# Performance work log

Hardware: AMD Instinct MI355X
Metric: run time of the kernel (lower is better)

The kernel has to match this reference:

```python
import jax, jax.numpy as jnp
import numpy as np

N = 100000
E = 1_600_000
IN = 128
HID = 32
HEADS = 4
OUT = 2
NEG_SLOPE = 0.2  # PyG GATv2Conv default negative_slope


def setup_inputs() -> dict:
    key = jax.random.key(0)
    ks = jax.random.split(key, 18)
    g = lambda k, shape, fan: jax.random.normal(k, shape, dtype=jnp.float32) / np.sqrt(fan)
    return {
        "x": jax.random.normal(ks[0], (N, IN), dtype=jnp.float32),
        "edge_index": jax.random.randint(ks[1], (2, E), 0, N, dtype=jnp.int32),
        # conv1: GATv2Conv(IN, HID, heads=HEADS)
        "W1l": g(ks[2], (IN, HEADS * HID), IN),
        "b1l": jnp.zeros((HEADS * HID,), jnp.float32),
        "W1r": g(ks[3], (IN, HEADS * HID), IN),
        "b1r": jnp.zeros((HEADS * HID,), jnp.float32),
        "att1": g(ks[4], (HEADS, HID), HID),
        "bias1": jnp.zeros((HEADS * HID,), jnp.float32),
        # conv2: GATv2Conv(HEADS*HID, HID, heads=1)
        "W2l": g(ks[5], (HEADS * HID, HID), HEADS * HID),
        "b2l": jnp.zeros((HID,), jnp.float32),
        "W2r": g(ks[6], (HEADS * HID, HID), HEADS * HID),
        "b2r": jnp.zeros((HID,), jnp.float32),
        "att2": g(ks[7], (1, HID), HID),
        "bias2": jnp.zeros((HID,), jnp.float32),
        # final linear
        "Wlin": g(ks[8], (HID, OUT), HID),
        "blin": jnp.zeros((OUT,), jnp.float32),
    }


def _gatv2(x, src, dst, Wl, bl, Wr, br, att, bias, heads, ch):
    n = x.shape[0]
    xl = (x @ Wl + bl).reshape(n, heads, ch)  # source transform
    xr = (x @ Wr + br).reshape(n, heads, ch)  # target transform
    # GATv2 edge score: a^T LeakyReLU(xl_j + xr_i)
    e = jax.nn.leaky_relu(xl[src] + xr[dst], NEG_SLOPE)      # [E, H, C]
    score = jnp.einsum('ehc,hc->eh', e, att)                  # [E, H]
    # segment softmax over edges sharing a destination node
    m = jax.ops.segment_max(score, dst, num_segments=n)
    ex = jnp.exp(score - m[dst])
    denom = jax.ops.segment_sum(ex, dst, num_segments=n)
    alpha = ex / denom[dst]                                   # [E, H]
    out = jax.ops.segment_sum(alpha[..., None] * xl[src], dst, num_segments=n)
    return out.reshape(n, heads * ch) + bias


def reference(x, edge_index, W1l, b1l, W1r, b1r, att1, bias1,
              W2l, b2l, W2r, b2r, att2, bias2, Wlin, blin):
    # add self-loops (PyG GATv2Conv default add_self_loops=True)
    loop = jnp.arange(N, dtype=edge_index.dtype)
    src = jnp.concatenate([edge_index[0], loop])
    dst = jnp.concatenate([edge_index[1], loop])

    h = _gatv2(x, src, dst, W1l, b1l, W1r, b1r, att1, bias1, HEADS, HID)
    h = jax.nn.elu(h)
    # dropout is inactive in eval mode
    h = _gatv2(h, src, dst, W2l, b2l, W2r, b2r, att2, bias2, 1, HID)
    h = jax.nn.elu(h)
    return h @ Wlin + blin  # [N, OUT]
```

## Files before the change

### kernel.cpp

```cpp
#include <hip/hip_runtime.h>
#include <hip/hip_fp16.h>
#include <math.h>

#define N_NODES 100000
#define E_EDGES 1600000
#define ETOT (E_EDGES + N_NODES)
#define NEG 0.2f
#define NB 782
#define BCAP 2560
#define CHUNK 8192
#define NCHB ((ETOT + CHUNK - 1) / CHUNK)
#define GEMM1_BLOCKS ((N_NODES + 63) / 64)

typedef _Float16 half8 __attribute__((ext_vector_type(8)));
typedef _Float16 half4v __attribute__((ext_vector_type(4)));
typedef _Float16 half2v __attribute__((ext_vector_type(2)));
typedef float floatx4 __attribute__((ext_vector_type(4)));

union H8I {
  half8 v;
  _Float16 e[8];
  int i[4];
};

__device__ __forceinline__ float elu(float v) { return v > 0.f ? v : (__expf(v) - 1.f); }

__device__ __forceinline__ float score8(half8 a, half8 r, half8 av) {
  half8 t = a + r;
  t = __builtin_elementwise_max(t, t * (_Float16)NEG);
  half8 s8 = t * av;
  half4v s4 = __builtin_shufflevector(s8, s8, 0, 1, 2, 3) +
              __builtin_shufflevector(s8, s8, 4, 5, 6, 7);
  half2v s2 = __builtin_shufflevector(s4, s4, 0, 1) +
              __builtin_shufflevector(s4, s4, 2, 3);
  return (float)s2[0] + (float)s2[1];
}

__global__ __launch_bounds__(256) void fusedA_kernel(
    const int* __restrict__ ei, unsigned* __restrict__ cursor,
    unsigned* __restrict__ bins,
    const float* __restrict__ W1l, const float* __restrict__ W1r,
    const float* __restrict__ b1l, const float* __restrict__ b1r,
    const float* __restrict__ W2l, const float* __restrict__ W2r,
    const float* __restrict__ b2l, const float* __restrict__ b2r,
    const float* __restrict__ att1, const float* __restrict__ att2,
    _Float16* __restrict__ Bperm, _Float16* __restrict__ B2perm,
    float* __restrict__ biascat, float* __restrict__ bias2cat,
    _Float16* __restrict__ att1h, _Float16* __restrict__ att2h) {
  int t = threadIdx.x;
  if (blockIdx.x < NCHB) {
    __shared__ unsigned cnt[NB];
    __shared__ unsigned base[NB];
    for (int b = t; b < NB; b += 256) cnt[b] = 0;
    __syncthreads();
    int e0 = blockIdx.x * CHUNK;
    int dstr[CHUNK / 256];
#pragma unroll
    for (int i = 0; i < CHUNK / 256; i++) {
      int e = e0 + i * 256 + t;
      int dst = 0;
      if (e < ETOT) {
        dst = (e < E_EDGES) ? ei[E_EDGES + e] : (e - E_EDGES);
        atomicAdd(&cnt[dst >> 7], 1u);
      }
      dstr[i] = dst;
    }
    __syncthreads();
    for (int b = t; b < NB; b += 256) {
      unsigned c = cnt[b];
      base[b] = c ? atomicAdd(&cursor[b], c) : 0u;
      cnt[b] = 0;
    }
    __syncthreads();
#pragma unroll
    for (int i = 0; i < CHUNK / 256; i++) {
      int e = e0 + i * 256 + t;
      if (e < ETOT) {
        int dst = dstr[i];
        int src = (e < E_EDGES) ? ei[e] : dst;
        int b = dst >> 7;
        unsigned off = atomicAdd(&cnt[b], 1u);
        bins[(size_t)b * BCAP + base[b] + off] =
            ((unsigned)(dst & 127) << 17) | (unsigned)src;
      }
    }
  } else {
    int pb = blockIdx.x - NCHB;
    int gt = pb * 256 + t;
    int gstr = 20 * 256;
    for (int e = gt; e < 4096; e += gstr) {
      int nt = e >> 8, kt = (e >> 6) & 3, lane = e & 63;
      int n = nt * 16 + (lane & 15);
      int kb = kt * 32 + (lane >> 4) * 8;
#pragma unroll
      for (int j = 0; j < 8; j++) {
        int k = kb + j;
        float val = (n < 128) ? W1l[k * 128 + n] : W1r[k * 128 + (n - 128)];
        Bperm[(size_t)e * 8 + j] = (_Float16)val;
      }
    }
    for (int e = gt; e < 1024; e += gstr) {
      int nt = e >> 8, kt = (e >> 6) & 3, lane = e & 63;
      int n = nt * 16 + (lane & 15);
      int kb = kt * 32 + (lane >> 4) * 8;
#pragma unroll
      for (int j = 0; j < 8; j++) {
        int k = kb + j;
        float val = (n < 32) ? W2l[k * 32 + n] : W2r[k * 32 + (n - 32)];
        B2perm[(size_t)e * 8 + j] = (_Float16)val;
      }
    }
    if (pb == 0) {
      biascat[t] = (t < 128) ? b1l[t] : b1r[t - 128];
      if (t < 64) bias2cat[t] = (t < 32) ? b2l[t] : b2r[t - 32];
      if (t < 128) att1h[t] = (_Float16)att1[t];
      if (t < 32) att2h[t] = (_Float16)att2[t];
    }
  }
}

__global__ __launch_bounds__(1024) void scan_buckets(const unsigned* __restrict__ cursor,
                                                     unsigned* __restrict__ bucket_base,
                                                     unsigned* __restrict__ rowptr) {
  __shared__ unsigned s[1024];
  int t = threadIdx.x;
  unsigned v = (t < NB) ? cursor[t] : 0u;
  s[t] = v;
  __syncthreads();
  for (int off = 1; off < 1024; off <<= 1) {
    unsigned a = (t >= off) ? s[t - off] : 0u;
    __syncthreads();
    s[t] += a;
    __syncthreads();
  }
  if (t < NB) bucket_base[t] = s[t] - v;
  if (t == 0) { bucket_base[NB] = ETOT; rowptr[N_NODES] = ETOT; }
}

__global__ __launch_bounds__(256) void fusedB_kernel(
    const unsigned* __restrict__ bins, const unsigned* __restrict__ cursor,
    const unsigned* __restrict__ bucket_base,
    unsigned* __restrict__ rowptr, int* __restrict__ csr_src,
    const float* __restrict__ x, const _Float16* __restrict__ Bperm,
    const float* __restrict__ biascat,
    __half* __restrict__ xlh, __half* __restrict__ xrh) {
  __shared__ __align__(16) char smem[64 * 256];
  int t = threadIdx.x;
  if (blockIdx.x < NB) {
    unsigned* cnt = (unsigned*)smem;
    unsigned* pref = cnt + 128;
    int b = blockIdx.x;
    unsigned cntb = cursor[b];
    unsigned bbase = bucket_base[b];
    const unsigned* bp = bins + (size_t)b * BCAP;
    if (t < 128) cnt[t] = 0;
    __syncthreads();
    for (unsigned i = t; i < cntb; i += 256) atomicAdd(&cnt[bp[i] >> 17], 1u);
    __syncthreads();
    if (t < 128) pref[t] = cnt[t];
    __syncthreads();
    for (int off = 1; off < 128; off <<= 1) {
      unsigned a = (t >= off && t < 128) ? pref[t - off] : 0u;
      __syncthreads();
      if (t < 128) pref[t] += a;
      __syncthreads();
    }
    if (t < 128) {
      unsigned excl = pref[t] - cnt[t];
      pref[t] = excl;
      int n = (b << 7) + t;
      if (n < N_NODES) rowptr[n] = bbase + excl;
      cnt[t] = 0;
    }
    __syncthreads();
    for (unsigned i = t; i < cntb; i += 256) {
      unsigned en = bp[i];
      int j = (int)(en >> 17);
      unsigned off = atomicAdd(&cnt[j], 1u);
      csr_src[bbase + pref[j] + off] = (int)(en & 0x1FFFFu);
    }
  } else {
    int base = (blockIdx.x - NB) * 64;
    {
      int row = t >> 2, c4 = t & 3;
      int grow = base + row;
      const float* gp = x + (size_t)grow * 128 + c4 * 32;
#pragma unroll
      for (int j = 0; j < 4; j++) {
        half8 v = {};
        if (grow < N_NODES) {
          float4 f0 = *(const float4*)(gp + j * 8);
          float4 f1 = *(const float4*)(gp + j * 8 + 4);
          v[0] = (_Float16)f0.x; v[1] = (_Float16)f0.y;
          v[2] = (_Float16)f0.z; v[3] = (_Float16)f0.w;
          v[4] = (_Float16)f1.x; v[5] = (_Float16)f1.y;
          v[6] = (_Float16)f1.z; v[7] = (_Float16)f1.w;
        }
        int off = row * 256 + ((((c4 * 4 + j) * 16)) ^ ((row & 7) << 4));
        *(half8*)(smem + off) = v;
      }
    }
    int wid = t >> 6, lane = t & 63;
    half8 bf[4][4];
#pragma unroll
    for (int ntl = 0; ntl < 4; ntl++)
#pragma unroll
      for (int kt = 0; kt < 4; kt++) {
        int f = (wid * 4 + ntl) * 4 + kt;
        bf[ntl][kt] = *(const half8*)(Bperm + ((size_t)f * 64 + lane) * 8);
      }
    floatx4 acc[4][4] = {};
    __syncthreads();
#pragma unroll
    for (int kt = 0; kt < 4; kt++) {
      half8 a[4];
#pragma unroll
      for (int mt = 0; mt < 4; mt++) {
        int row = mt * 16 + (lane & 15);
        int kchunk = kt * 4 + (lane >> 4);
        int off = row * 256 + ((kchunk * 16) ^ ((row & 7) << 4));
        a[mt] = *(const half8*)(smem + off);
      }
#pragma unroll
      for (int mt = 0; mt < 4; mt++)
#pragma unroll
        for (int ntl = 0; ntl < 4; ntl++)
          acc[mt][ntl] = __builtin_amdgcn_mfma_f32_16x16x32_f16(a[mt], bf[ntl][kt],
                                                                acc[mt][ntl], 0, 0, 0);
    }
#pragma unroll
    for (int mt = 0; mt < 4; mt++) {
#pragma unroll
      for (int i = 0; i < 4; i++) {
        int row = base + mt * 16 + (lane >> 4) * 4 + i;
        if (row >= N_NODES) continue;
#pragma unroll
        for (int ntl = 0; ntl < 4; ntl++) {
          int col = wid * 64 + ntl * 16 + (lane & 15);
          float v = acc[mt][ntl][i] + biascat[col];
          if (col < 128) xlh[(size_t)row * 128 + col] = __float2half_rn(v);
          else xrh[(size_t)row * 128 + (col - 128)] = __float2half_rn(v);
        }
      }
    }
  }
}

__global__ __launch_bounds__(256) void gemm2_mfma(
    const __half* __restrict__ h1h, const _Float16* __restrict__ B2perm,
    const float* __restrict__ bias2cat,
    __half* __restrict__ xl2h, __half* __restrict__ xr2h) {
  __shared__ __align__(16) char smem[64 * 256];
  int t = threadIdx.x;
  int base = blockIdx.x * 64;
  {
    int row = t >> 2, c4 = t & 3;
    int grow = base + row;
    const char* gp = (const char*)(h1h + (size_t)grow * 128 + c4 * 32);
#pragma unroll
    for (int j = 0; j < 4; j++) {
      half8 v = {};
      if (grow < N_NODES) v = *(const half8*)(gp + j * 16);
      int off = row * 256 + ((((c4 * 4 + j) * 16)) ^ ((row & 7) << 4));
      *(half8*)(smem + off) = v;
    }
  }
  int wid = t >> 6, lane = t & 63;
  half8 bf[4];
#pragma unroll
  for (int kt = 0; kt < 4; kt++) {
    int f = wid * 4 + kt;
    bf[kt] = *(const half8*)(B2perm + ((size_t)f * 64 + lane) * 8);
  }
  floatx4 acc[4] = {};
  __syncthreads();
#pragma unroll
  for (int kt = 0; kt < 4; kt++) {
    half8 a[4];
#pragma unroll
    for (int mt = 0; mt < 4; mt++) {
      int row = mt * 16 + (lane & 15);
      int kchunk = kt * 4 + (lane >> 4);
      int off = row * 256 + ((kchunk * 16) ^ ((row & 7) << 4));
      a[mt] = *(const half8*)(smem + off);
    }
#pragma unroll
    for (int mt = 0; mt < 4; mt++)
      acc[mt] = __builtin_amdgcn_mfma_f32_16x16x32_f16(a[mt], bf[kt], acc[mt], 0, 0, 0);
  }
  int col = wid * 16 + (lane & 15);
  float bv = bias2cat[col];
#pragma unroll
  for (int mt = 0; mt < 4; mt++) {
#pragma unroll
    for (int i = 0; i < 4; i++) {
      int row = base + mt * 16 + (lane >> 4) * 4 + i;
      if (row >= N_NODES) continue;
      float v = acc[mt][i] + bv;
      if (col < 32) xl2h[(size_t)row * 32 + col] = __float2half_rn(v);
      else xr2h[(size_t)row * 32 + (col - 32)] = __float2half_rn(v);
    }
  }
}

__global__ __launch_bounds__(256) void l1_gather_kernel(
    const __half* __restrict__ xlh, const __half* __restrict__ xrh,
    const int* __restrict__ csr_src, const unsigned* __restrict__ rowptr,
    const _Float16* __restrict__ att1h, const float* __restrict__ bias,
    __half* __restrict__ h1h) {
  int wid = threadIdx.x >> 6;
  int lane = threadIdx.x & 63;
  int n = blockIdx.x * 4 + wid;
  if (n >= N_NODES) return;
  int g = lane >> 4;
  int q = lane & 15;
  int c0 = q * 8;
  half8 rv = *(const half8*)(xrh + (size_t)n * 128 + c0);
  half8 av = *(const half8*)(att1h + c0);
  unsigned beg = rowptr[n], end = rowptr[n + 1];
  int nit = (int)(end - beg + 3) >> 2;
  float d = 0.f;
  H8I acc;
  acc.v = (half8){};
  for (int i = 0; i < nit; i++) {
    unsigned e = beg + i * 4 + g;
    bool valid = e < end;
    int s = csr_src[valid ? e : (end - 1)];
    H8I a;
    a.v = *(const half8*)(xlh + (size_t)s * 128 + c0);
    float v = score8(a.v, rv, av);
    v += __shfl_xor(v, 1);
    v += __shfl_xor(v, 2);
    float p = valid ? __expf(v - 4.f) : 0.f;
    d += p;
    _Float16 ph = (_Float16)p;
    half8 p8 = {ph, ph, ph, ph, ph, ph, ph, ph};
    acc.v = p8 * a.v + acc.v;
  }
#pragma unroll
  for (int msk = 16; msk <= 32; msk <<= 1) {
    d += __shfl_xor(d, msk);
    H8I o;
#pragma unroll
    for (int k = 0; k < 4; k++) o.i[k] = __shfl_xor(acc.i[k], msk);
    acc.v = acc.v + o.v;
  }
  if (g == 0) {
    float inv = 1.f / d;
    H8I res;
#pragma unroll
    for (int j = 0; j < 8; j++)
      res.e[j] = (_Float16)elu((float)acc.e[j] * inv + bias[c0 + j]);
    *(half8*)(h1h + (size_t)n * 128 + c0) = res.v;
  }
}

__global__ __launch_bounds__(256) void l2_gather_kernel(
    const __half* __restrict__ xl2h, const __half* __restrict__ xr2h,
    const int* __restrict__ csr_src, const unsigned* __restrict__ rowptr,
    const _Float16* __restrict__ att2h, const float* __restrict__ bias,
    const float* __restrict__ Wlin, const float* __restrict__ blin,
    float* __restrict__ out) {
  int wid = threadIdx.x >> 6;
  int lane = threadIdx.x & 63;
  int n = blockIdx.x * 4 + wid;
  if (n >= N_NODES) return;
  int g = lane >> 2;
  int q = lane & 3;
  int c0 = q * 8;
  half8 rv = *(const half8*)(xr2h + (size_t)n * 32 + c0);
  half8 av = *(const half8*)(att2h + c0);
  unsigned beg = rowptr[n], end = rowptr[n + 1];
  int nit = (int)(end - beg + 15) >> 4;
  float d = 0.f;
  H8I acc;
  acc.v = (half8){};
  for (int i = 0; i < nit; i++) {
    unsigned e = beg + i * 16 + g;
    bool valid = e < end;
    int s = csr_src[valid ? e : (end - 1)];
    H8I a;
    a.v = *(const half8*)(xl2h + (size_t)s * 32 + c0);
    float v = score8(a.v, rv, av);
    v += __shfl_xor(v, 1);
    v += __shfl_xor(v, 2);
    float p = valid ? __expf(v - 4.f) : 0.f;
    d += p;
    _Float16 ph = (_Float16)p;
    half8 p8 = {ph, ph, ph, ph, ph, ph, ph, ph};
    acc.v = p8 * a.v + acc.v;
  }
#pragma unroll
  for (int msk = 4; msk <= 32; msk <<= 1) {
    d += __shfl_xor(d, msk);
    H8I o;
#pragma unroll
    for (int k = 0; k < 4; k++) o.i[k] = __shfl_xor(acc.i[k], msk);
    acc.v = acc.v + o.v;
  }
  float inv = 1.f / d;
  float o0 = 0.f, o1 = 0.f;
#pragma unroll
  for (int j = 0; j < 8; j++) {
    float v = elu((float)acc.e[j] * inv + bias[c0 + j]);
    o0 = fmaf(v, Wlin[(c0 + j) * 2 + 0], o0);
    o1 = fmaf(v, Wlin[(c0 + j) * 2 + 1], o1);
  }
  o0 += __shfl_xor(o0, 1); o1 += __shfl_xor(o1, 1);
  o0 += __shfl_xor(o0, 2); o1 += __shfl_xor(o1, 2);
  if (lane == 0) {
    out[(size_t)n * 2 + 0] = o0 + blin[0];
    out[(size_t)n * 2 + 1] = o1 + blin[1];
  }
}

extern "C" void kernel_launch(void* const* d_in, const int* in_sizes, int n_in,
                              void* d_out, int out_size, void* d_ws, size_t ws_size,
                              hipStream_t stream) {
  const float* x     = (const float*)d_in[0];
  const int*   ei    = (const int*)d_in[1];
  const float* W1l   = (const float*)d_in[2];
  const float* b1l   = (const float*)d_in[3];
  const float* W1r   = (const float*)d_in[4];
  const float* b1r   = (const float*)d_in[5];
  const float* att1  = (const float*)d_in[6];
  const float* bias1 = (const float*)d_in[7];
  const float* W2l   = (const float*)d_in[8];
  const float* b2l   = (const float*)d_in[9];
  const float* W2r   = (const float*)d_in[10];
  const float* b2r   = (const float*)d_in[11];
  const float* att2  = (const float*)d_in[12];
  const float* bias2 = (const float*)d_in[13];
  const float* Wlin  = (const float*)d_in[14];
  const float* blin  = (const float*)d_in[15];
  float* out = (float*)d_out;

  __half* xl1h  = (__half*)d_ws;
  __half* xr1h  = xl1h + (size_t)N_NODES * 128;
  __half* h1h   = xr1h + (size_t)N_NODES * 128;
  __half* xl2h  = h1h + (size_t)N_NODES * 128;
  __half* xr2h  = xl2h + (size_t)N_NODES * 32;
  _Float16* Bperm  = (_Float16*)(xr2h + (size_t)N_NODES * 32);
  _Float16* B2perm = Bperm + 32768;
  _Float16* att1h  = B2perm + 8192;
  _Float16* att2h  = att1h + 128;
  float* biascat   = (float*)(att2h + 32);
  float* bias2cat  = biascat + 256;
  int* csr_src     = (int*)(bias2cat + 64);
  unsigned* rowptr = (unsigned*)(csr_src + (size_t)ETOT);
  unsigned* cursor = rowptr + (N_NODES + 1);
  unsigned* bucket_base = cursor + NB;
  unsigned* bins   = bucket_base + NB + 1;

  (void)hipMemsetAsync(cursor, 0, (size_t)NB * sizeof(unsigned), stream);
  fusedA_kernel<<<NCHB + 20, 256, 0, stream>>>(
      ei, cursor, bins, W1l, W1r, b1l, b1r, W2l, W2r, b2l, b2r, att1, att2,
      Bperm, B2perm, biascat, bias2cat, att1h, att2h);
  scan_buckets<<<1, 1024, 0, stream>>>(cursor, bucket_base, rowptr);
  fusedB_kernel<<<NB + GEMM1_BLOCKS, 256, 0, stream>>>(
      bins, cursor, bucket_base, rowptr, csr_src, x, Bperm, biascat, xl1h, xr1h);

  l1_gather_kernel<<<(N_NODES + 3) / 4, 256, 0, stream>>>(
      (const __half*)xl1h, (const __half*)xr1h, csr_src, rowptr, att1h, bias1, h1h);

  gemm2_mfma<<<GEMM1_BLOCKS, 256, 0, stream>>>(h1h, B2perm, bias2cat, xl2h, xr2h);
  l2_gather_kernel<<<(N_NODES + 3) / 4, 256, 0, stream>>>(
      xl2h, xr2h, csr_src, rowptr, att2h, bias2, Wlin, blin, out);
}
```

Baseline: 251.5 us.

## Replicate bucket cursors, synthesize self-loops directly, and split gather loops into full/remainder

Result: faster. 238.3 us (-5.2%).

```diff
diff --git a/kernel.cpp b/kernel.cpp
--- a/kernel.cpp
+++ b/kernel.cpp
@@ -7,9 +7,11 @@
 #define ETOT (E_EDGES + N_NODES)
 #define NEG 0.2f
 #define NB 782
-#define BCAP 2560
-#define CHUNK 8192
-#define NCHB ((ETOT + CHUNK - 1) / CHUNK)
+#define NREP 4
+#define SEG 704
+#define BCAP (NREP * SEG)
+#define CHUNK 4096
+#define NCHB ((E_EDGES + CHUNK - 1) / CHUNK)
 #define GEMM1_BLOCKS ((N_NODES + 63) / 64)
 
 typedef _Float16 half8 __attribute__((ext_vector_type(8)));
@@ -51,6 +53,7 @@
   if (blockIdx.x < NCHB) {
     __shared__ unsigned cnt[NB];
     __shared__ unsigned base[NB];
+    int rep = blockIdx.x & (NREP - 1);
     for (int b = t; b < NB; b += 256) cnt[b] = 0;
     __syncthreads();
     int e0 = blockIdx.x * CHUNK;
@@ -59,8 +62,8 @@
     for (int i = 0; i < CHUNK / 256; i++) {
       int e = e0 + i * 256 + t;
       int dst = 0;
-      if (e < ETOT) {
-        dst = (e < E_EDGES) ? ei[E_EDGES + e] : (e - E_EDGES);
+      if (e < E_EDGES) {
+        dst = ei[E_EDGES + e];
         atomicAdd(&cnt[dst >> 7], 1u);
       }
       dstr[i] = dst;
@@ -68,19 +71,19 @@
     __syncthreads();
     for (int b = t; b < NB; b += 256) {
       unsigned c = cnt[b];
-      base[b] = c ? atomicAdd(&cursor[b], c) : 0u;
+      base[b] = c ? atomicAdd(&cursor[rep * NB + b], c) : 0u;
       cnt[b] = 0;
     }
     __syncthreads();
 #pragma unroll
     for (int i = 0; i < CHUNK / 256; i++) {
       int e = e0 + i * 256 + t;
-      if (e < ETOT) {
+      if (e < E_EDGES) {
         int dst = dstr[i];
-        int src = (e < E_EDGES) ? ei[e] : dst;
+        int src = ei[e];
         int b = dst >> 7;
         unsigned off = atomicAdd(&cnt[b], 1u);
-        bins[(size_t)b * BCAP + base[b] + off] =
+        bins[(size_t)b * BCAP + rep * SEG + base[b] + off] =
             ((unsigned)(dst & 127) << 17) | (unsigned)src;
       }
     }
@@ -124,7 +127,13 @@
                                                      unsigned* __restrict__ rowptr) {
   __shared__ unsigned s[1024];
   int t = threadIdx.x;
-  unsigned v = (t < NB) ? cursor[t] : 0u;
+  unsigned v = 0;
+  if (t < NB) {
+#pragma unroll
+    for (int r = 0; r < NREP; r++) v += cursor[r * NB + t];
+    int nib = N_NODES - (t << 7);
+    v += (nib > 128) ? 128u : (unsigned)nib;
+  }
   s[t] = v;
   __syncthreads();
   for (int off = 1; off < 1024; off <<= 1) {
@@ -150,14 +159,21 @@
     unsigned* cnt = (unsigned*)smem;
     unsigned* pref = cnt + 128;
     int b = blockIdx.x;
-    unsigned cntb = cursor[b];
+    int nib = N_NODES - (b << 7);
+    if (nib > 128) nib = 128;
     unsigned bbase = bucket_base[b];
+    unsigned crs[NREP];
+#pragma unroll
+    for (int r = 0; r < NREP; r++) crs[r] = cursor[r * NB + b];
     const unsigned* bp = bins + (size_t)b * BCAP;
     if (t < 128) cnt[t] = 0;
     __syncthreads();
-    for (unsigned i = t; i < cntb; i += 256) atomicAdd(&cnt[bp[i] >> 17], 1u);
-    __syncthreads();
-    if (t < 128) pref[t] = cnt[t];
+#pragma unroll
+    for (int r = 0; r < NREP; r++)
+      for (unsigned i = t; i < crs[r]; i += 256)
+        atomicAdd(&cnt[bp[r * SEG + i] >> 17], 1u);
+    __syncthreads();
+    if (t < 128) pref[t] = (t < nib) ? cnt[t] + 1u : 0u;
     __syncthreads();
     for (int off = 1; off < 128; off <<= 1) {
       unsigned a = (t >= off && t < 128) ? pref[t - off] : 0u;
@@ -166,19 +182,25 @@
       __syncthreads();
     }
     if (t < 128) {
-      unsigned excl = pref[t] - cnt[t];
+      unsigned tot = (t < nib) ? cnt[t] + 1u : 0u;
+      unsigned excl = pref[t] - tot;
       pref[t] = excl;
-      int n = (b << 7) + t;
-      if (n < N_NODES) rowptr[n] = bbase + excl;
+      if (t < nib) {
+        int n = (b << 7) + t;
+        rowptr[n] = bbase + excl;
+        csr_src[bbase + excl] = n;
+      }
       cnt[t] = 0;
     }
     __syncthreads();
-    for (unsigned i = t; i < cntb; i += 256) {
-      unsigned en = bp[i];
-      int j = (int)(en >> 17);
-      unsigned off = atomicAdd(&cnt[j], 1u);
-      csr_src[bbase + pref[j] + off] = (int)(en & 0x1FFFFu);
-    }
+#pragma unroll
+    for (int r = 0; r < NREP; r++)
+      for (unsigned i = t; i < crs[r]; i += 256) {
+        unsigned en = bp[r * SEG + i];
+        int j = (int)(en >> 17);
+        unsigned off = atomicAdd(&cnt[j], 1u);
+        csr_src[bbase + pref[j] + 1u + off] = (int)(en & 0x1FFFFu);
+      }
   } else {
     int base = (blockIdx.x - NB) * 64;
     {
@@ -318,14 +340,28 @@
   half8 rv = *(const half8*)(xrh + (size_t)n * 128 + c0);
   half8 av = *(const half8*)(att1h + c0);
   unsigned beg = rowptr[n], end = rowptr[n + 1];
-  int nit = (int)(end - beg + 3) >> 2;
+  unsigned deg = end - beg;
+  unsigned nfull = deg >> 2, rem = deg & 3;
   float d = 0.f;
   H8I acc;
   acc.v = (half8){};
-  for (int i = 0; i < nit; i++) {
-    unsigned e = beg + i * 4 + g;
-    bool valid = e < end;
-    int s = csr_src[valid ? e : (end - 1)];
+  unsigned e = beg + g;
+  for (unsigned i = 0; i < nfull; i++, e += 4) {
+    int s = csr_src[e];
+    H8I a;
+    a.v = *(const half8*)(xlh + (size_t)s * 128 + c0);
+    float v = score8(a.v, rv, av);
+    v += __shfl_xor(v, 1);
+    v += __shfl_xor(v, 2);
+    float p = __expf(v - 4.f);
+    d += p;
+    _Float16 ph = (_Float16)p;
+    half8 p8 = {ph, ph, ph, ph, ph, ph, ph, ph};
+    acc.v = p8 * a.v + acc.v;
+  }
+  if (rem) {
+    bool valid = (unsigned)g < rem;
+    int s = csr_src[valid ? e : beg];
     H8I a;
     a.v = *(const half8*)(xlh + (size_t)s * 128 + c0);
     float v = score8(a.v, rv, av);
@@ -371,14 +407,28 @@
   half8 rv = *(const half8*)(xr2h + (size_t)n * 32 + c0);
   half8 av = *(const half8*)(att2h + c0);
   unsigned beg = rowptr[n], end = rowptr[n + 1];
-  int nit = (int)(end - beg + 15) >> 4;
+  unsigned deg = end - beg;
+  unsigned nfull = deg >> 4, rem = deg & 15;
   float d = 0.f;
   H8I acc;
   acc.v = (half8){};
-  for (int i = 0; i < nit; i++) {
-    unsigned e = beg + i * 16 + g;
-    bool valid = e < end;
-    int s = csr_src[valid ? e : (end - 1)];
+  unsigned e = beg + g;
+  for (unsigned i = 0; i < nfull; i++, e += 16) {
+    int s = csr_src[e];
+    H8I a;
+    a.v = *(const half8*)(xl2h + (size_t)s * 32 + c0);
+    float v = score8(a.v, rv, av);
+    v += __shfl_xor(v, 1);
+    v += __shfl_xor(v, 2);
+    float p = __expf(v - 4.f);
+    d += p;
+    _Float16 ph = (_Float16)p;
+    half8 p8 = {ph, ph, ph, ph, ph, ph, ph, ph};
+    acc.v = p8 * a.v + acc.v;
+  }
+  if (rem) {
+    bool valid = (unsigned)g < rem;
+    int s = csr_src[valid ? e : beg];
     H8I a;
     a.v = *(const half8*)(xl2h + (size_t)s * 32 + c0);
     float v = score8(a.v, rv, av);
@@ -449,10 +499,10 @@
   int* csr_src     = (int*)(bias2cat + 64);
   unsigned* rowptr = (unsigned*)(csr_src + (size_t)ETOT);
   unsigned* cursor = rowptr + (N_NODES + 1);
-  unsigned* bucket_base = cursor + NB;
+  unsigned* bucket_base = cursor + NREP * NB;
   unsigned* bins   = bucket_base + NB + 1;
 
-  (void)hipMemsetAsync(cursor, 0, (size_t)NB * sizeof(unsigned), stream);
+  (void)hipMemsetAsync(cursor, 0, (size_t)NREP * NB * sizeof(unsigned), stream);
   fusedA_kernel<<<NCHB + 20, 256, 0, stream>>>(
       ei, cursor, bins, W1l, W1r, b1l, b1r, W2l, W2r, b2l, b2r, att1, att2,
       Bperm, B2perm, biascat, bias2cat, att1h, att2h);
```
